# Performance work log

Hardware: AMD Instinct MI355X
Metric: run time of the kernel (lower is better)

The kernel has to match this reference:

```python
import jax, jax.numpy as jnp
import numpy as np

G, S, M = 4, 2048, 1024   # groups (batch), tokens per group, emb dim
E, H, K = 8, 4096, 2      # experts, mlp dim, top-k
CAP = int(K * S / E * 1.25)  # expert capacity = 640
AUX_COEF, Z_COEF = 0.01, 0.001


def setup_inputs() -> dict:
    key = jax.random.key(0)
    k1, k2, k3, k4, k5 = jax.random.split(key, 5)
    return {
        "inputs": jax.random.normal(k1, (G, S, M), jnp.float32),
        "paddings": jnp.zeros((G, S), jnp.float32),  # 1.0 = padded token
        "router_w": jax.random.normal(k2, (M, E), jnp.float32) / np.sqrt(M),
        "wi_gate": jax.random.normal(k3, (E, M, H), jnp.float32) / np.sqrt(M),
        "wi_0": jax.random.normal(k4, (E, M, H), jnp.float32) / np.sqrt(M),
        "wo": jax.random.normal(k5, (E, H, M), jnp.float32) / np.sqrt(H),
    }


def reference(inputs, paddings, router_w, wi_gate, wi_0, wo):
    # Router
    logits = jnp.einsum('gsm,me->gse', inputs, router_w)          # [G,S,E]
    probs = jax.nn.softmax(logits, axis=-1)
    top_p, top_i = jax.lax.top_k(probs, K)                        # [G,S,K]

    nonpad = 1.0 - paddings                                       # [G,S]
    exp_mask = jax.nn.one_hot(top_i, E, dtype=jnp.float32)        # [G,S,K,E]
    exp_mask = exp_mask * nonpad[:, :, None, None]

    # Position in expert (capacity-limited), priority by token order then k slot
    mask_flat = exp_mask.reshape(G, S * K, E)
    pos = jnp.cumsum(mask_flat, axis=1) * mask_flat               # 1-indexed where assigned
    keep = mask_flat * (pos <= CAP)
    pos_oh = jax.nn.one_hot((pos - 1.0).astype(jnp.int32), CAP, dtype=jnp.float32)  # [G,SK,E,CAP]
    dispatch_k = (keep[..., None] * pos_oh).reshape(G, S, K, E, CAP)
    dispatch = dispatch_k.sum(axis=2)                             # [G,S,E,CAP]
    combine = jnp.einsum('gsk,gskec->gsec', top_p, dispatch_k)    # [G,S,E,CAP]

    # Dispatch -> gated expert FFN -> combine
    expert_in = jnp.einsum('gsec,gsm->egcm', dispatch, inputs)    # [E,G,CAP,M]
    h = jax.nn.silu(jnp.einsum('egcm,emh->egch', expert_in, wi_gate)) \
        * jnp.einsum('egcm,emh->egch', expert_in, wi_0)           # [E,G,CAP,H]
    expert_out = jnp.einsum('egch,ehm->egcm', h, wo)              # [E,G,CAP,M]
    output = jnp.einsum('gsec,egcm->gsm', combine, expert_out)    # [G,S,M]

    # Aux losses: load-balancing (Switch style) + router z-loss
    em = jnp.max(jax.nn.one_hot(top_i, E, dtype=jnp.float32), axis=-2)       # [G,S,E]
    lb = jnp.mean(jnp.mean(em, axis=-2) * jnp.mean(probs, axis=-2)) * E * E
    z = jnp.mean(jax.nn.logsumexp(logits, axis=-1) ** 2)
    aux_loss = AUX_COEF * lb + Z_COEF * z
    return output, aux_loss
```

## Files before the change

### kernel.cpp

```cpp
#include <hip/hip_runtime.h>
#include <hip/hip_bf16.h>
#include <math.h>

#define G 4
#define S 2048
#define MDIM 1024
#define E 8
#define HDIM 4096
#define TOPK 2
#define CAP 640
#define GC (G*CAP)

typedef __attribute__((ext_vector_type(8))) short bf16x8;
typedef __attribute__((ext_vector_type(4))) short s16x4;
typedef __attribute__((ext_vector_type(4))) float f32x4;
typedef unsigned int u32;
typedef unsigned short u16;

#define MFMA16(a,b,c) __builtin_amdgcn_mfma_f32_16x16x32_bf16(a,b,c,0,0,0)

__device__ __forceinline__ u16 f2bf(float f) {
    union { float f; u32 u; } v; v.f = f;
    u32 r = v.u + 0x7fffu + ((v.u >> 16) & 1u);
    return (u16)(r >> 16);
}

__device__ __forceinline__ void gload16(const char* gp, char* lp) {
    __builtin_amdgcn_global_load_lds((const __attribute__((address_space(1))) u32*)gp,
                                     (__attribute__((address_space(3))) u32*)lp,
                                     16, 0, 0);
}

__device__ __forceinline__ int swzb(int r) { return ((r >> 1) & 3) << 4; }

__global__ __launch_bounds__(256) void transpose_cvt(const float* __restrict__ in,
                                                     u16* __restrict__ out, int R, int C) {
    int e = blockIdx.z;
    const float* ine = in + (size_t)e * R * C;
    u16* oute = out + (size_t)e * R * C;
    __shared__ float tile[32][33];
    int tx = threadIdx.x, ty = threadIdx.y;
    int x0 = blockIdx.x * 32, y0 = blockIdx.y * 32;
    #pragma unroll
    for (int i = 0; i < 4; ++i)
        tile[ty + i*8][tx] = ine[(size_t)(y0 + ty + i*8) * C + x0 + tx];
    __syncthreads();
    #pragma unroll
    for (int i = 0; i < 4; ++i)
        oute[(size_t)(x0 + ty + i*8) * R + y0 + tx] = f2bf(tile[tx][ty + i*8]);
}

__global__ __launch_bounds__(256) void router_kernel(const float* __restrict__ inp,
                                                     const float* __restrict__ rw,
                                                     int* __restrict__ top_i,
                                                     float* __restrict__ top_p,
                                                     float* __restrict__ partials) {
    int wid = threadIdx.x >> 6, lane = threadIdx.x & 63;
    int tok = blockIdx.x * 4 + wid;
    const float* x = inp + (size_t)tok * MDIM;
    float acc[E] = {0.f,0.f,0.f,0.f,0.f,0.f,0.f,0.f};
    #pragma unroll
    for (int rep = 0; rep < 4; ++rep) {
        int m0 = rep * 256 + lane * 4;
        f32x4 xv = *(const f32x4*)(x + m0);
        #pragma unroll
        for (int j = 0; j < 4; ++j) {
            const float* r = rw + (size_t)(m0 + j) * E;
            float xj = xv[j];
            #pragma unroll
            for (int e = 0; e < E; ++e) acc[e] += xj * r[e];
        }
    }
    #pragma unroll
    for (int e = 0; e < E; ++e)
        #pragma unroll
        for (int off = 32; off; off >>= 1) acc[e] += __shfl_down(acc[e], off);

    __shared__ float part[4][17];
    if (lane == 0) {
        float mx = acc[0];
        #pragma unroll
        for (int e = 1; e < E; ++e) mx = fmaxf(mx, acc[e]);
        float p[E], sum = 0.f;
        #pragma unroll
        for (int e = 0; e < E; ++e) { p[e] = expf(acc[e] - mx); sum += p[e]; }
        float inv = 1.f / sum;
        #pragma unroll
        for (int e = 0; e < E; ++e) p[e] *= inv;
        float lse = logf(sum) + mx;
        int i0 = 0;
        #pragma unroll
        for (int e = 1; e < E; ++e) if (acc[e] > acc[i0]) i0 = e;
        int i1 = (i0 == 0) ? 1 : 0;
        #pragma unroll
        for (int e = 0; e < E; ++e) if (e != i0 && acc[e] > acc[i1]) i1 = e;
        top_i[tok*2+0] = i0; top_i[tok*2+1] = i1;
        top_p[tok*2+0] = p[i0]; top_p[tok*2+1] = p[i1];
        #pragma unroll
        for (int e = 0; e < E; ++e) { part[wid][e] = p[e]; part[wid][8+e] = 0.f; }
        part[wid][8+i0] = 1.f; part[wid][8+i1] = 1.f;
        part[wid][16] = lse * lse;
    }
    __syncthreads();
    if (threadIdx.x < 17) {
        float v = part[0][threadIdx.x] + part[1][threadIdx.x] +
                  part[2][threadIdx.x] + part[3][threadIdx.x];
        partials[(size_t)blockIdx.x * 17 + threadIdx.x] = v;
    }
}

__global__ __launch_bounds__(256) void reduce_partials(const float* __restrict__ partials,
                                                       float* __restrict__ sums) {
    int g = blockIdx.x, t = threadIdx.x;
    float loc[17];
    #pragma unroll
    for (int c = 0; c < 17; ++c) loc[c] = 0.f;
    for (int r = t; r < 1024; r += 256) {
        const float* pr = partials + ((size_t)g * 1024 + r) * 17;
        #pragma unroll
        for (int c = 0; c < 17; ++c) loc[c] += pr[c];
    }
    __shared__ float red[256];
    for (int c = 0; c < 17; ++c) {
        red[t] = loc[c]; __syncthreads();
        for (int off = 128; off; off >>= 1) {
            if (t < off) red[t] += red[t + off];
            __syncthreads();
        }
        if (t == 0) sums[g * 17 + c] = red[0];
        __syncthreads();
    }
}

__global__ void aux_final(const float* __restrict__ sums, float* __restrict__ out) {
    float lb = 0.f, z = 0.f;
    for (int g = 0; g < G; ++g) {
        for (int e = 0; e < E; ++e)
            lb += (sums[g*17 + 8 + e] / (float)S) * (sums[g*17 + e] / (float)S);
        z += sums[g*17 + 16];
    }
    lb = lb / (float)(G * E) * (float)(E * E);
    z /= (float)(G * S);
    out[(size_t)G * S * MDIM] = 0.01f * lb + 0.001f * z;
}

__global__ __launch_bounds__(256) void scan_kernel(const int* __restrict__ top_i,
                                                   const float* __restrict__ pad,
                                                   int* __restrict__ slot_token,
                                                   int* __restrict__ token_c) {
    int b = blockIdx.x; int g = b >> 3, e = b & 7;
    int t = threadIdx.x;
    __shared__ int sums[256];
    int base = t * 16;
    int run = 0; unsigned mask16 = 0; int loc[16];
    #pragma unroll
    for (int j = 0; j < 16; ++j) {
        int i = base + j; int s = i >> 1, k = i & 1;
        int ex = top_i[((size_t)(g * S + s)) * 2 + k];
        int m = (ex == e) && (pad[g * S + s] == 0.f);
        run += m; loc[j] = run; mask16 |= ((unsigned)m << j);
    }
    sums[t] = run; __syncthreads();
    for (int off = 1; off < 256; off <<= 1) {
        int v = (t >= off) ? sums[t - off] : 0;
        __syncthreads();
        sums[t] += v;
        __syncthreads();
    }
    int excl = sums[t] - run;
    #pragma unroll
    for (int j = 0; j < 16; ++j) {
        if ((mask16 >> j) & 1u) {
            int pos = excl + loc[j];
            if (pos <= CAP) {
                int i = base + j; int s = i >> 1, k = i & 1;
                slot_token[((size_t)(e * G + g)) * CAP + (pos - 1)] = s;
                token_c[((size_t)(g * S + s)) * 2 + k] = pos - 1;
            }
        }
    }
}

__global__ __launch_bounds__(128) void gather_kernel(const float* __restrict__ inp,
                                                     const int* __restrict__ slot_token,
                                                     u16* __restrict__ X) {
    int row = blockIdx.x;
    int t = threadIdx.x;
    int s = slot_token[row];
    int g = (row % GC) / CAP;
    bf16x8 v;
    if (s >= 0) {
        const float* src = inp + ((size_t)(g * S + s)) * MDIM + t * 8;
        f32x4 a = *(const f32x4*)src;
        f32x4 b = *(const f32x4*)(src + 4);
        #pragma unroll
        for (int j = 0; j < 4; ++j) { v[j] = (short)f2bf(a[j]); v[4+j] = (short)f2bf(b[j]); }
    } else {
        #pragma unroll
        for (int j = 0; j < 8; ++j) v[j] = 0;
    }
    *(bf16x8*)(X + (size_t)row * MDIM + t * 8) = v;
}

__global__ __launch_bounds__(512, 1) void gemm_ffn12_v4(
        const u16* __restrict__ Xb, const u16* __restrict__ WgT,
        const u16* __restrict__ W0T, u16* __restrict__ Hb) {
    extern __shared__ char smem[];
    const int NK = MDIM / 32;
    int bid = blockIdx.x;
    int swz = (bid & 7) * 320 + (bid >> 3);
    int mt = swz % 10, nt = (swz / 10) & 31, e = swz / 320;
    const char* A  = (const char*)(Xb  + (size_t)e * GC * MDIM   + (size_t)mt * 256 * MDIM);
    const char* Bg = (const char*)(WgT + (size_t)e * HDIM * MDIM + (size_t)nt * 128 * MDIM);
    const char* B0 = (const char*)(W0T + (size_t)e * HDIM * MDIM + (size_t)nt * 128 * MDIM);
    int tid = threadIdx.x, w = tid >> 6, l = tid & 63;
    int wm = w >> 2, wn = w & 3;
    int rl = l >> 2, cch = (l & 3) * 16;
    int fr = l & 15, fg = l >> 4;
    int lswz = ((fr >> 1) & 3) << 4;

    int rA0 = (0 * 8 + w) * 16 + rl, rA1 = (1 * 8 + w) * 16 + rl, rB = w * 16 + rl;
    const char* gA0 = A  + (size_t)rA0 * MDIM * 2 + (cch ^ swzb(rA0));
    const char* gA1 = A  + (size_t)rA1 * MDIM * 2 + (cch ^ swzb(rA1));
    const char* gBg = Bg + (size_t)rB  * MDIM * 2 + (cch ^ swzb(rB));
    const char* gB0 = B0 + (size_t)rB  * MDIM * 2 + (cch ^ swzb(rB));
    int baseA = (wm * 128 + fr) * 64 + ((fg * 16) ^ lswz);
    int baseB = (wn * 32  + fr) * 64 + ((fg * 16) ^ lswz);

    f32x4 ag[8][2], ao[8][2];
    #pragma unroll
    for (int i = 0; i < 8; ++i) {
        ag[i][0] = (f32x4){0,0,0,0}; ag[i][1] = (f32x4){0,0,0,0};
        ao[i][0] = (f32x4){0,0,0,0}; ao[i][1] = (f32x4){0,0,0,0};
    }

    auto stage = [&](int tt) {
        int kk = tt * 64, b = tt & 3;
        gload16(gA0 + kk, smem + b * 16384 + (0 * 8 + w) * 1024);
        gload16(gA1 + kk, smem + b * 16384 + (1 * 8 + w) * 1024);
        gload16(gBg + kk, smem + 65536 + b * 8192 + w * 1024);
        gload16(gB0 + kk, smem + 98304 + b * 8192 + w * 1024);
    };

    stage(0); stage(1);

    #pragma unroll 1
    for (int t = 0; t < NK; ++t) {
        if (t + 2 < NK) {
            stage(t + 2);
            asm volatile("s_waitcnt vmcnt(4)" ::: "memory");
        } else {
            asm volatile("s_waitcnt vmcnt(0)" ::: "memory");
        }
        __builtin_amdgcn_s_barrier();
        __builtin_amdgcn_sched_barrier(0);
        const char* bufA = smem + (t & 3) * 16384;
        const char* pG = smem + 65536 + (t & 3) * 8192 + baseB;
        const char* pO = smem + 98304 + (t & 3) * 8192 + baseB;
        bf16x8 bgf[2], bof[2], af[8];
        bgf[0] = *(const bf16x8*)(pG);  bgf[1] = *(const bf16x8*)(pG + 1024);
        bof[0] = *(const bf16x8*)(pO);  bof[1] = *(const bf16x8*)(pO + 1024);
        #pragma unroll
        for (int fm = 0; fm < 8; ++fm) af[fm] = *(const bf16x8*)(bufA + baseA + fm * 1024);
        __builtin_amdgcn_s_setprio(1);
        #pragma unroll
        for (int fm = 0; fm < 8; ++fm)
            #pragma unroll
            for (int fn = 0; fn < 2; ++fn) {
                ag[fm][fn] = MFMA16(bgf[fn], af[fm], ag[fm][fn]);
                ao[fm][fn] = MFMA16(bof[fn], af[fm], ao[fm][fn]);
            }
        __builtin_amdgcn_s_setprio(0);
    }

    u16* He = Hb + (size_t)e * GC * HDIM;
    int row0 = mt * 256 + wm * 128 + fr;
    int col0 = nt * 128 + wn * 32 + fg * 4;
    #pragma unroll
    for (int fm = 0; fm < 8; ++fm)
        #pragma unroll
        for (int fn = 0; fn < 2; ++fn) {
            s16x4 pk;
            #pragma unroll
            for (int r = 0; r < 4; ++r) {
                float gv = ag[fm][fn][r], ov = ao[fm][fn][r];
                float hv = gv / (1.f + __expf(-gv)) * ov;
                pk[r] = (short)f2bf(hv);
            }
            *(s16x4*)(He + (size_t)(row0 + fm * 16) * HDIM + col0 + fn * 16) = pk;
        }
}

__global__ __launch_bounds__(512, 1) void gemm_out_v4(
        const u16* __restrict__ Hb, const u16* __restrict__ WoT,
        float* __restrict__ EO) {
    extern __shared__ char smem[];
    const int NK = HDIM / 32;
    int bid = blockIdx.x;
    int swz = (bid & 7) * 80 + (bid >> 3);
    int nt = swz & 3, mt = (swz / 4) % 20, e = swz / 80;
    const char* A = (const char*)(Hb  + (size_t)e * GC * HDIM   + (size_t)mt * 128 * HDIM);
    const char* B = (const char*)(WoT + (size_t)e * MDIM * HDIM + (size_t)nt * 256 * HDIM);
    int tid = threadIdx.x, w = tid >> 6, l = tid & 63;
    int wm = w >> 2, wn = w & 3;
    int rl = l >> 2, cch = (l & 3) * 16;
    int fr = l & 15, fg = l >> 4;
    int lswz = ((fr >> 1) & 3) << 4;

    int rA = w * 16 + rl, rB0 = (0 * 8 + w) * 16 + rl, rB1 = (1 * 8 + w) * 16 + rl;
    const char* gA  = A + (size_t)rA  * HDIM * 2 + (cch ^ swzb(rA));
    const char* gBa = B + (size_t)rB0 * HDIM * 2 + (cch ^ swzb(rB0));
    const char* gBb = B + (size_t)rB1 * HDIM * 2 + (cch ^ swzb(rB1));
    int baseA = (wm * 64 + fr) * 64 + ((fg * 16) ^ lswz);
    int baseB = (wn * 64 + fr) * 64 + ((fg * 16) ^ lswz);

    f32x4 acc[4][4];
    #pragma unroll
    for (int i = 0; i < 4; ++i)
        #pragma unroll
        for (int j = 0; j < 4; ++j) acc[i][j] = (f32x4){0,0,0,0};

    auto stage = [&](int tt) {
        int kk = tt * 64, b = tt & 3;
        gload16(gA  + kk, smem + b * 8192 + w * 1024);
        gload16(gBa + kk, smem + 32768 + b * 16384 + (0 * 8 + w) * 1024);
        gload16(gBb + kk, smem + 32768 + b * 16384 + (1 * 8 + w) * 1024);
    };

    bf16x8 afA[4], bfA[4], afB[4], bfB[4];

    stage(0); stage(1);
    asm volatile("s_waitcnt vmcnt(3)" ::: "memory");
    __builtin_amdgcn_s_barrier();
    __builtin_amdgcn_sched_barrier(0);
    {
        const char* pA = smem + baseA;
        const char* pB = smem + 32768 + baseB;
        #pragma unroll
        for (int i = 0; i < 4; ++i) {
            afA[i] = *(const bf16x8*)(pA + i * 1024);
            bfA[i] = *(const bf16x8*)(pB + i * 1024);
        }
    }

    auto body = [&](int t, bf16x8 (&afc)[4], bf16x8 (&bfc)[4],
                    bf16x8 (&afn)[4], bf16x8 (&bfn)[4]) {
        if (t + 2 < NK) {
            stage(t + 2);
            asm volatile("s_waitcnt vmcnt(3)" ::: "memory");
        } else {
            asm volatile("s_waitcnt vmcnt(0)" ::: "memory");
        }
        __builtin_amdgcn_s_barrier();
        __builtin_amdgcn_sched_barrier(0);
        if (t + 1 < NK) {
            const char* pA = smem + ((t + 1) & 3) * 8192 + baseA;
            const char* pB = smem + 32768 + ((t + 1) & 3) * 16384 + baseB;
            #pragma unroll
            for (int i = 0; i < 4; ++i) {
                afn[i] = *(const bf16x8*)(pA + i * 1024);
                bfn[i] = *(const bf16x8*)(pB + i * 1024);
            }
        }
        __builtin_amdgcn_s_setprio(1);
        #pragma unroll
        for (int fm = 0; fm < 4; ++fm)
            #pragma unroll
            for (int fn = 0; fn < 4; ++fn)
                acc[fm][fn] = MFMA16(bfc[fn], afc[fm], acc[fm][fn]);
        __builtin_amdgcn_s_setprio(0);
    };

    #pragma unroll 1
    for (int t = 0; t < NK; t += 2) {
        body(t, afA, bfA, afB, bfB);
        body(t + 1, afB, bfB, afA, bfA);
    }

    float* Ee = EO + (size_t)e * GC * MDIM;
    int row0 = mt * 128 + wm * 64 + fr;
    int col0 = nt * 256 + wn * 64 + fg * 4;
    #pragma unroll
    for (int fm = 0; fm < 4; ++fm)
        #pragma unroll
        for (int fn = 0; fn < 4; ++fn)
            *(f32x4*)(Ee + (size_t)(row0 + fm * 16) * MDIM + col0 + fn * 16) = acc[fm][fn];
}

__global__ __launch_bounds__(256) void combine_kernel(const float* __restrict__ EO,
                                                      const int* __restrict__ top_i,
                                                      const float* __restrict__ top_p,
                                                      const int* __restrict__ token_c,
                                                      float* __restrict__ out) {
    int tok = blockIdx.x, t = threadIdx.x;
    int g = tok >> 11;
    f32x4 acc = {0.f, 0.f, 0.f, 0.f};
    #pragma unroll
    for (int k = 0; k < 2; ++k) {
        int c = token_c[tok * 2 + k];
        if (c >= 0) {
            int e = top_i[tok * 2 + k];
            float p = top_p[tok * 2 + k];
            const float* src = EO + ((size_t)e * GC + g * CAP + c) * MDIM + t * 4;
            f32x4 v = *(const f32x4*)src;
            #pragma unroll
            for (int j = 0; j < 4; ++j) acc[j] += p * v[j];
        }
    }
    *(f32x4*)(out + (size_t)tok * MDIM + t * 4) = acc;
}

extern "C" void kernel_launch(void* const* d_in, const int* in_sizes, int n_in,
                              void* d_out, int out_size, void* d_ws, size_t ws_size,
                              hipStream_t stream) {
    (void)in_sizes; (void)n_in; (void)out_size; (void)ws_size;
    const float* inputs   = (const float*)d_in[0];
    const float* paddings = (const float*)d_in[1];
    const float* router_w = (const float*)d_in[2];
    const float* wi_gate  = (const float*)d_in[3];
    const float* wi_0     = (const float*)d_in[4];
    const float* wo       = (const float*)d_in[5];
    float* out = (float*)d_out;

    char* p = (char*)d_ws;
    u16* WgT = (u16*)p; p += (size_t)E * HDIM * MDIM * 2;
    u16* W0T = (u16*)p; p += (size_t)E * HDIM * MDIM * 2;
    u16* WoT = (u16*)p; p += (size_t)E * HDIM * MDIM * 2;
    u16* Xb  = (u16*)p; p += (size_t)E * GC * MDIM * 2;
    u16* Hb  = (u16*)p; p += (size_t)E * GC * HDIM * 2;
    float* EO = (float*)p; p += (size_t)E * GC * MDIM * 4;
    int*   top_i = (int*)p;   p += (size_t)G * S * TOPK * 4;
    float* top_p = (float*)p; p += (size_t)G * S * TOPK * 4;
    int*   token_c = (int*)p; p += (size_t)G * S * TOPK * 4;
    int*   slot_token = (int*)p; p += (size_t)E * G * CAP * 4;
    float* partials = (float*)p; p += (size_t)4096 * 17 * 4;
    float* sums = (float*)p; p += 4 * 17 * 4;

    hipMemsetAsync(token_c, 0xFF, (size_t)G * S * TOPK * 4, stream);
    hipMemsetAsync(slot_token, 0xFF, (size_t)E * G * CAP * 4, stream);

    hipFuncSetAttribute((const void*)gemm_ffn12_v4,
                        hipFuncAttributeMaxDynamicSharedMemorySize, 131072);
    hipFuncSetAttribute((const void*)gemm_out_v4,
                        hipFuncAttributeMaxDynamicSharedMemorySize, 98304);

    transpose_cvt<<<dim3(HDIM/32, MDIM/32, E), dim3(32, 8), 0, stream>>>(wi_gate, WgT, MDIM, HDIM);
    transpose_cvt<<<dim3(HDIM/32, MDIM/32, E), dim3(32, 8), 0, stream>>>(wi_0,   W0T, MDIM, HDIM);
    transpose_cvt<<<dim3(MDIM/32, HDIM/32, E), dim3(32, 8), 0, stream>>>(wo,     WoT, HDIM, MDIM);

    router_kernel<<<G * S / 4, 256, 0, stream>>>(inputs, router_w, top_i, top_p, partials);
    reduce_partials<<<G, 256, 0, stream>>>(partials, sums);
    scan_kernel<<<G * E, 256, 0, stream>>>(top_i, paddings, slot_token, token_c);
    gather_kernel<<<E * GC, 128, 0, stream>>>(inputs, slot_token, Xb);
    gemm_ffn12_v4<<<2560, 512, 131072, stream>>>(Xb, WgT, W0T, Hb);
    gemm_out_v4<<<640, 512, 98304, stream>>>(Hb, WoT, EO);
    combine_kernel<<<G * S, 256, 0, stream>>>(EO, top_i, top_p, token_c, out);
    aux_final<<<1, 1, 0, stream>>>(sums, out);
}
```

Baseline: 802.5 us.

## Prefetch next-step A fragments in FFN GEMM and vectorize weight transpose

The gate/up GEMM loop is unrolled by two and now loads the first half of the A fragments for the next k-step from LDS during the current step. This overlaps LDS read latency with MFMA work, at the cost of extra registers. The weight transpose-convert kernel moves to 64x64 tiles, with 16-byte float loads and packed 4-element bf16 stores, to improve memory efficiency. The padded LDS tile may still see some bank conflicts on the column reads.

Result: no change. 796.8 us (-0.7%).

```diff
diff --git a/kernel.cpp b/kernel.cpp
--- a/kernel.cpp
+++ b/kernel.cpp
@@ -38,16 +38,25 @@
     int e = blockIdx.z;
     const float* ine = in + (size_t)e * R * C;
     u16* oute = out + (size_t)e * R * C;
-    __shared__ float tile[32][33];
-    int tx = threadIdx.x, ty = threadIdx.y;
-    int x0 = blockIdx.x * 32, y0 = blockIdx.y * 32;
-    #pragma unroll
-    for (int i = 0; i < 4; ++i)
-        tile[ty + i*8][tx] = ine[(size_t)(y0 + ty + i*8) * C + x0 + tx];
+    __shared__ float tile[64][68];
+    int t = threadIdx.x;
+    int x0 = blockIdx.x * 64, y0 = blockIdx.y * 64;
+    int lx = (t & 15) * 4, ly = t >> 4;
+    #pragma unroll
+    for (int i = 0; i < 4; ++i) {
+        f32x4 v = *(const f32x4*)(ine + (size_t)(y0 + ly + i * 16) * C + x0 + lx);
+        *(f32x4*)&tile[ly + i * 16][lx] = v;
+    }
     __syncthreads();
-    #pragma unroll
-    for (int i = 0; i < 4; ++i)
-        oute[(size_t)(x0 + ty + i*8) * R + y0 + tx] = f2bf(tile[tx][ty + i*8]);
+    int rr0 = (t & 15) * 4, cb = t >> 4;
+    #pragma unroll
+    for (int p = 0; p < 4; ++p) {
+        int cc = cb + p * 16;
+        s16x4 pk;
+        #pragma unroll
+        for (int j = 0; j < 4; ++j) pk[j] = (short)f2bf(tile[rr0 + j][cc]);
+        *(s16x4*)(oute + (size_t)(x0 + cc) * R + y0 + rr0) = pk;
+    }
 }
 
 __global__ __launch_bounds__(256) void router_kernel(const float* __restrict__ inp,
@@ -202,7 +211,7 @@
     *(bf16x8*)(X + (size_t)row * MDIM + t * 8) = v;
 }
 
-__global__ __launch_bounds__(512, 1) void gemm_ffn12_v4(
+__global__ __launch_bounds__(512, 1) void gemm_ffn12_v5(
         const u16* __restrict__ Xb, const u16* __restrict__ WgT,
         const u16* __restrict__ W0T, u16* __restrict__ Hb) {
     extern __shared__ char smem[];
@@ -242,10 +251,19 @@
         gload16(gB0 + kk, smem + 98304 + b * 8192 + w * 1024);
     };
 
+    bf16x8 afL0[4], afL1[4];
+
     stage(0); stage(1);
-
-    #pragma unroll 1
-    for (int t = 0; t < NK; ++t) {
+    asm volatile("s_waitcnt vmcnt(4)" ::: "memory");
+    __builtin_amdgcn_s_barrier();
+    __builtin_amdgcn_sched_barrier(0);
+    {
+        const char* p0 = smem + baseA;
+        #pragma unroll
+        for (int i = 0; i < 4; ++i) afL0[i] = *(const bf16x8*)(p0 + i * 1024);
+    }
+
+    auto body = [&](int t, bf16x8 (&loC)[4], bf16x8 (&loN)[4]) {
         if (t + 2 < NK) {
             stage(t + 2);
             asm volatile("s_waitcnt vmcnt(4)" ::: "memory");
@@ -254,23 +272,41 @@
         }
         __builtin_amdgcn_s_barrier();
         __builtin_amdgcn_sched_barrier(0);
-        const char* bufA = smem + (t & 3) * 16384;
         const char* pG = smem + 65536 + (t & 3) * 8192 + baseB;
         const char* pO = smem + 98304 + (t & 3) * 8192 + baseB;
-        bf16x8 bgf[2], bof[2], af[8];
+        bf16x8 bgf[2], bof[2], hi[4];
         bgf[0] = *(const bf16x8*)(pG);  bgf[1] = *(const bf16x8*)(pG + 1024);
         bof[0] = *(const bf16x8*)(pO);  bof[1] = *(const bf16x8*)(pO + 1024);
-        #pragma unroll
-        for (int fm = 0; fm < 8; ++fm) af[fm] = *(const bf16x8*)(bufA + baseA + fm * 1024);
+        const char* bufA = smem + (t & 3) * 16384 + baseA;
+        #pragma unroll
+        for (int i = 0; i < 4; ++i) hi[i] = *(const bf16x8*)(bufA + (4 + i) * 1024);
+        if (t + 1 < NK) {
+            const char* bufN = smem + ((t + 1) & 3) * 16384 + baseA;
+            #pragma unroll
+            for (int i = 0; i < 4; ++i) loN[i] = *(const bf16x8*)(bufN + i * 1024);
+        }
         __builtin_amdgcn_s_setprio(1);
         #pragma unroll
-        for (int fm = 0; fm < 8; ++fm)
+        for (int fm = 0; fm < 4; ++fm)
             #pragma unroll
             for (int fn = 0; fn < 2; ++fn) {
-                ag[fm][fn] = MFMA16(bgf[fn], af[fm], ag[fm][fn]);
-                ao[fm][fn] = MFMA16(bof[fn], af[fm], ao[fm][fn]);
+                ag[fm][fn] = MFMA16(bgf[fn], loC[fm], ag[fm][fn]);
+                ao[fm][fn] = MFMA16(bof[fn], loC[fm], ao[fm][fn]);
+            }
+        #pragma unroll
+        for (int fm = 0; fm < 4; ++fm)
+            #pragma unroll
+            for (int fn = 0; fn < 2; ++fn) {
+                ag[4+fm][fn] = MFMA16(bgf[fn], hi[fm], ag[4+fm][fn]);
+                ao[4+fm][fn] = MFMA16(bof[fn], hi[fm], ao[4+fm][fn]);
             }
         __builtin_amdgcn_s_setprio(0);
+    };
+
+    #pragma unroll 1
+    for (int t = 0; t < NK; t += 2) {
+        body(t, afL0, afL1);
+        body(t + 1, afL1, afL0);
     }
 
     u16* He = Hb + (size_t)e * GC * HDIM;
@@ -439,20 +475,20 @@
     hipMemsetAsync(token_c, 0xFF, (size_t)G * S * TOPK * 4, stream);
     hipMemsetAsync(slot_token, 0xFF, (size_t)E * G * CAP * 4, stream);
 
-    hipFuncSetAttribute((const void*)gemm_ffn12_v4,
+    hipFuncSetAttribute((const void*)gemm_ffn12_v5,
                         hipFuncAttributeMaxDynamicSharedMemorySize, 131072);
     hipFuncSetAttribute((const void*)gemm_out_v4,
                         hipFuncAttributeMaxDynamicSharedMemorySize, 98304);
 
-    transpose_cvt<<<dim3(HDIM/32, MDIM/32, E), dim3(32, 8), 0, stream>>>(wi_gate, WgT, MDIM, HDIM);
-    transpose_cvt<<<dim3(HDIM/32, MDIM/32, E), dim3(32, 8), 0, stream>>>(wi_0,   W0T, MDIM, HDIM);
-    transpose_cvt<<<dim3(MDIM/32, HDIM/32, E), dim3(32, 8), 0, stream>>>(wo,     WoT, HDIM, MDIM);
+    transpose_cvt<<<dim3(HDIM/64, MDIM/64, E), 256, 0, stream>>>(wi_gate, WgT, MDIM, HDIM);
+    transpose_cvt<<<dim3(HDIM/64, MDIM/64, E), 256, 0, stream>>>(wi_0,   W0T, MDIM, HDIM);
+    transpose_cvt<<<dim3(MDIM/64, HDIM/64, E), 256, 0, stream>>>(wo,     WoT, HDIM, MDIM);
 
     router_kernel<<<G * S / 4, 256, 0, stream>>>(inputs, router_w, top_i, top_p, partials);
     reduce_partials<<<G, 256, 0, stream>>>(partials, sums);
     scan_kernel<<<G * E, 256, 0, stream>>>(top_i, paddings, slot_token, token_c);
     gather_kernel<<<E * GC, 128, 0, stream>>>(inputs, slot_token, Xb);
-    gemm_ffn12_v4<<<2560, 512, 131072, stream>>>(Xb, WgT, W0T, Hb);
+    gemm_ffn12_v5<<<2560, 512, 131072, stream>>>(Xb, WgT, W0T, Hb);
     gemm_out_v4<<<640, 512, 98304, stream>>>(Hb, WoT, EO);
     combine_kernel<<<G * S, 256, 0, stream>>>(EO, top_i, top_p, token_c, out);
     aux_final<<<1, 1, 0, stream>>>(sums, out);
```
